# Kernel optimization log

Measured on AMD Instinct MI355X. Metric: run time of the kernel, lower is better.

Reference implementation:

```python
import jax, jax.numpy as jnp
from jax import lax
import numpy as np

# pywt db4 reconstruction lowpass filter (rec_lo); rec_hi derived by QMF relation
DB4_REC_LO = np.array([0.23037781330885523, 0.7148465705525415, 0.6308807679295904,
                       -0.02798376941698385, -0.18703481171888114, 0.030841381835986965,
                       0.032883011666982945, -0.010597401784997278], dtype=np.float32)


def _filters():
    g0 = jnp.asarray(DB4_REC_LO)
    L = g0.shape[0]
    # pywt orthogonal QMF: rec_hi[k] = (-1)^k * rec_lo[L-1-k]
    g1 = ((-1.0) ** jnp.arange(L, dtype=jnp.float32)) * g0[::-1]
    return g0, g1


def _sfb1d(lo, hi, g0, g1, axis):
    """1D synthesis filter bank along `axis`, mode='zero'.
    Equivalent to torch conv_transpose(stride=2, padding=L-2): out_len = 2n - L + 2.
    Implemented as lhs-dilated correlation with the flipped kernel, pad (1,1)."""
    L = g0.shape[0]
    lo = jnp.moveaxis(lo, axis, -1)
    hi = jnp.moveaxis(hi, axis, -1)
    shp = lo.shape
    x0 = lo.reshape(-1, 1, shp[-1])
    x1 = hi.reshape(-1, 1, shp[-1])
    k0 = g0[::-1].reshape(1, 1, L)
    k1 = g1[::-1].reshape(1, 1, L)
    dn = ('NCH', 'OIH', 'NCH')
    y = (lax.conv_general_dilated(x0, k0, (1,), [(1, 1)], lhs_dilation=(2,), dimension_numbers=dn)
         + lax.conv_general_dilated(x1, k1, (1,), [(1, 1)], lhs_dilation=(2,), dimension_numbers=dn))
    y = y.reshape(shp[:-1] + (y.shape[-1],))
    return jnp.moveaxis(y, -1, axis)


def _sfb3d(low, highs, g0, g1):
    # band index bits (bH, bW, bD); band 0 is the lowpass `low`, bands 1..7 from `highs`
    bands = [low] + [highs[:, :, i] for i in range(7)]
    # synthesize along depth (last axis)
    t = [_sfb1d(bands[2 * j], bands[2 * j + 1], g0, g1, -1) for j in range(4)]
    # then along rows (W)
    t = [_sfb1d(t[2 * j], t[2 * j + 1], g0, g1, -2) for j in range(2)]
    # then along cols (H)
    return _sfb1d(t[0], t[1], g0, g1, -3)


def setup_inputs() -> dict:
    key = jax.random.key(0)
    k1, k2, k3 = jax.random.split(key, 3)
    yl = jax.random.normal(k1, (2, 8, 36, 36, 36), dtype=jnp.float32)
    yh0 = jax.random.normal(k2, (2, 8, 7, 66, 66, 66), dtype=jnp.float32)
    yh1 = jax.random.normal(k3, (2, 8, 7, 36, 36, 36), dtype=jnp.float32)
    return {"yl": yl, "yh0": yh0, "yh1": yh1}


def reference(yl, yh0, yh1):
    g0, g1 = _filters()
    ll = yl
    for h in (yh1, yh0):  # coarsest level first (yh reversed)
        # crop ll if one larger than the highpass bands (odd-size handling)
        ll = ll[..., :h.shape[-3], :, :]
        ll = ll[..., :h.shape[-2], :]
        ll = ll[..., :h.shape[-1]]
        ll = _sfb3d(ll, h, g0, g1)
    return ll
```

## Files before the change

kernel.cpp:

```cpp
#include <hip/hip_runtime.h>

__device__ constexpr float G0[8] = {
    0.23037781330885523f,  0.7148465705525415f,  0.6308807679295904f,  -0.02798376941698385f,
    -0.18703481171888114f, 0.030841381835986965f, 0.032883011666982945f, -0.010597401784997278f};
__device__ constexpr float G1[8] = {
    -0.010597401784997278f, -0.032883011666982945f, 0.030841381835986965f, 0.18703481171888114f,
    -0.02798376941698385f,  -0.6308807679295904f,   0.7148465705525415f,  -0.23037781330885523f};

template <int n, int WY>
__global__ __launch_bounds__(256) void idwt3_lds(const float* __restrict__ low,
                                                 const float* __restrict__ highs,
                                                 float* __restrict__ out) {
  constexpr int N = 2 * n - 6;
  constexpr int H = N / 2;
  constexpr int ROWS = WY + 3;
  constexpr int REAL4 = (ROWS * n + 3) / 4;
  constexpr int CH = 4 * REAL4;
  constexpr int TOT4 = 5 * REAL4;
  constexpr int K = (TOT4 + 255) / 256;
  constexpr long n3 = (long)n * n * n;
  constexpr int n3_4 = (int)(n3 / 4);

  __shared__ __align__(16) float slab[5 * CH];

  const int tid = threadIdx.x;
  const int zb0 = blockIdx.x * 2;
  const int yb0 = blockIdx.y * WY;
  const int b = blockIdx.z;
  const int ux = tid % H;
  const int ty = tid / H;
  const bool z1ok = (zb0 + 1) < H;

  const float* const lowv = low + (long)b * n3;
  const float* const highv = highs + (long)b * 7 * n3;

  float4 st[K];

  auto stage_load = [&](int band) {
    const float* src = (band == 0) ? lowv : (highv + (long)(band - 1) * n3);
#pragma unroll
    for (int k = 0; k < K; ++k) {
      const int idx = tid + k * 256;
      if (idx < TOT4) {
        const int dv = idx / REAL4;
        const int c = idx - dv * REAL4;
        const int v = min(zb0 + dv, n - 1);
        int rel4 = ((v * n + yb0) * n) / 4 + c;
        rel4 = min(rel4, n3_4 - 1);
        st[k] = *reinterpret_cast<const float4*>(src + 4 * (long)rel4);
      }
    }
  };

  float acc[4][2][2] = {};

  stage_load(0);

#pragma unroll 1
  for (int band = 0; band < 8; ++band) {
    if (band) __syncthreads();
#pragma unroll
    for (int k = 0; k < K; ++k) {
      const int idx = tid + k * 256;
      if (idx < TOT4) *reinterpret_cast<float4*>(&slab[4 * idx]) = st[k];
    }
    __syncthreads();
    if (band < 7) stage_load(band + 1);

    if (ty < WY) {
      const float* Gx = (band & 1) ? G1 : G0;
      const float* Gy = (band & 2) ? G1 : G0;
      const float* Gz = (band & 4) ? G1 : G0;
#pragma unroll
      for (int dv = 0; dv < 5; ++dv) {
        float d[4][2];
#pragma unroll
        for (int du = 0; du < 4; ++du) {
          const int base = dv * CH + (ty + du) * n + ux;
          const float r0 = slab[base], r1 = slab[base + 1];
          const float r2 = slab[base + 2], r3 = slab[base + 3];
          d[du][0] = r3 * Gx[0] + r2 * Gx[2] + r1 * Gx[4] + r0 * Gx[6];
          d[du][1] = r3 * Gx[1] + r2 * Gx[3] + r1 * Gx[5] + r0 * Gx[7];
        }
        float ey[2][2];
#pragma unroll
        for (int py = 0; py < 2; ++py) {
#pragma unroll
          for (int px = 0; px < 2; ++px) {
            float s = d[0][px] * Gy[py + 6];
            s = fmaf(d[1][px], Gy[py + 4], s);
            s = fmaf(d[2][px], Gy[py + 2], s);
            s = fmaf(d[3][px], Gy[py + 0], s);
            ey[py][px] = s;
          }
        }
#pragma unroll
        for (int zo = 0; zo < 4; ++zo) {
          const int mz = (zo >> 1) + 3 - dv;
          if (mz >= 0 && mz <= 3) {
            const float w = Gz[(zo & 1) + 2 * mz];
#pragma unroll
            for (int py = 0; py < 2; ++py)
#pragma unroll
              for (int px = 0; px < 2; ++px)
                acc[zo][py][px] = fmaf(ey[py][px], w, acc[zo][py][px]);
          }
        }
      }
    }
  }

  const int uy = yb0 + ty;
  if (ty < WY && uy < H) {
    const long N3 = (long)N * N * N;
    float* obase = out + (long)b * N3 + 2 * ux;
#pragma unroll
    for (int zo = 0; zo < 4; ++zo) {
      if (zo >= 2 && !z1ok) continue;
      const int gz = 2 * zb0 + zo;
#pragma unroll
      for (int py = 0; py < 2; ++py) {
        const int gy = 2 * uy + py;
        float2 vv = make_float2(acc[zo][py][0], acc[zo][py][1]);
        *reinterpret_cast<float2*>(obase + ((long)gz * N + gy) * N) = vv;
      }
    }
  }
}

extern "C" void kernel_launch(void* const* d_in, const int* in_sizes, int n_in,
                              void* d_out, int out_size, void* d_ws, size_t ws_size,
                              hipStream_t stream) {
  const float* yl  = nullptr;
  const float* yh0 = nullptr;
  const float* yh1 = nullptr;
  for (int i = 0; i < n_in; ++i) {
    if (in_sizes[i] == 746496)        yl  = (const float*)d_in[i];
    else if (in_sizes[i] == 32199552) yh0 = (const float*)d_in[i];
    else if (in_sizes[i] == 5225472)  yh1 = (const float*)d_in[i];
  }
  if (!yl || !yh0 || !yh1) {
    yl  = (const float*)d_in[0];
    yh0 = (const float*)d_in[1];
    yh1 = (const float*)d_in[2];
  }
  float* out = (float*)d_out;
  float* ll  = (float*)d_ws;

  idwt3_lds<36, 7><<<dim3(17, 5, 16), 256, 0, stream>>>(yl, yh1, ll);

  idwt3_lds<66, 4><<<dim3(32, 16, 16), 256, 0, stream>>>(ll, yh0, out);
}
```

Measured before the change: 516.6 us.

## Separate x-axis synthesis into shared pass pairing lo/hi bands

Bands are now handled in lo/hi pairs along x. A cooperative pass filters each pair along x into a shared intermediate buffer, and the y/z passes then read that buffer instead of redoing the x filter per band. This removes the x-filter work that was repeated for every output row and halves the number of outer band iterations. In exchange it doubles register staging and shared-memory use, which can lower occupancy, and adds an extra barrier per pair. The first-level launch also changes row tiling from 7 to 3 rows per block with more blocks.

```diff
diff --git a/kernel.cpp b/kernel.cpp
--- a/kernel.cpp
+++ b/kernel.cpp
@@ -8,20 +8,25 @@
     -0.02798376941698385f,  -0.6308807679295904f,   0.7148465705525415f,  -0.23037781330885523f};
 
 template <int n, int WY>
-__global__ __launch_bounds__(256) void idwt3_lds(const float* __restrict__ low,
+__global__ __launch_bounds__(256) void idwt3_sep(const float* __restrict__ low,
                                                  const float* __restrict__ highs,
                                                  float* __restrict__ out) {
   constexpr int N = 2 * n - 6;
   constexpr int H = N / 2;
   constexpr int ROWS = WY + 3;
-  constexpr int REAL4 = (ROWS * n + 3) / 4;
+  constexpr int CHF = ROWS * n;
+  constexpr int REAL4 = (CHF + 3) / 4;
   constexpr int CH = 4 * REAL4;
   constexpr int TOT4 = 5 * REAL4;
   constexpr int K = (TOT4 + 255) / 256;
+  constexpr int W2 = 2 * H;
+  constexpr int PTOT = 5 * ROWS * H;
+  constexpr int KX = (PTOT + 255) / 256;
   constexpr long n3 = (long)n * n * n;
   constexpr int n3_4 = (int)(n3 / 4);
 
-  __shared__ __align__(16) float slab[5 * CH];
+  __shared__ __align__(16) float raw[2][5 * CH];
+  __shared__ __align__(16) float xs[5 * ROWS * W2];
 
   const int tid = threadIdx.x;
   const int zb0 = blockIdx.x * 2;
@@ -34,10 +39,11 @@
   const float* const lowv = low + (long)b * n3;
   const float* const highv = highs + (long)b * 7 * n3;
 
-  float4 st[K];
+  float4 st[2][K];
 
-  auto stage_load = [&](int band) {
-    const float* src = (band == 0) ? lowv : (highv + (long)(band - 1) * n3);
+  auto stage_load = [&](int p) {
+    const float* srcL = (p == 0) ? lowv : (highv + (long)(2 * p - 1) * n3);
+    const float* srcH = highv + (long)(2 * p) * n3;
 #pragma unroll
     for (int k = 0; k < K; ++k) {
       const int idx = tid + k * 256;
@@ -47,7 +53,8 @@
         const int v = min(zb0 + dv, n - 1);
         int rel4 = ((v * n + yb0) * n) / 4 + c;
         rel4 = min(rel4, n3_4 - 1);
-        st[k] = *reinterpret_cast<const float4*>(src + 4 * (long)rel4);
+        st[0][k] = *reinterpret_cast<const float4*>(srcL + 4 * (long)rel4);
+        st[1][k] = *reinterpret_cast<const float4*>(srcH + 4 * (long)rel4);
       }
     }
   };
@@ -57,30 +64,53 @@
   stage_load(0);
 
 #pragma unroll 1
-  for (int band = 0; band < 8; ++band) {
-    if (band) __syncthreads();
+  for (int p = 0; p < 4; ++p) {
 #pragma unroll
     for (int k = 0; k < K; ++k) {
       const int idx = tid + k * 256;
-      if (idx < TOT4) *reinterpret_cast<float4*>(&slab[4 * idx]) = st[k];
+      if (idx < TOT4) {
+        *reinterpret_cast<float4*>(&raw[0][4 * idx]) = st[0][k];
+        *reinterpret_cast<float4*>(&raw[1][4 * idx]) = st[1][k];
+      }
     }
     __syncthreads();
-    if (band < 7) stage_load(band + 1);
+    if (p < 3) stage_load(p + 1);
+
+#pragma unroll
+    for (int k = 0; k < KX; ++k) {
+      const int idx = tid + k * 256;
+      if (idx < PTOT) {
+        const int dv = idx / (ROWS * H);
+        const int r = idx - dv * (ROWS * H);
+        const int row = r / H;
+        const int u = r - row * H;
+        const int base = dv * CH + row * n + u;
+        const float l0 = raw[0][base],     l1 = raw[0][base + 1],
+                    l2 = raw[0][base + 2], l3 = raw[0][base + 3];
+        const float h0 = raw[1][base],     h1 = raw[1][base + 1],
+                    h2 = raw[1][base + 2], h3 = raw[1][base + 3];
+        float x0 = l0 * G0[6] + l1 * G0[4] + l2 * G0[2] + l3 * G0[0]
+                 + h0 * G1[6] + h1 * G1[4] + h2 * G1[2] + h3 * G1[0];
+        float x1 = l0 * G0[7] + l1 * G0[5] + l2 * G0[3] + l3 * G0[1]
+                 + h0 * G1[7] + h1 * G1[5] + h2 * G1[3] + h3 * G1[1];
+        *reinterpret_cast<float2*>(&xs[(dv * ROWS + row) * W2 + 2 * u]) =
+            make_float2(x0, x1);
+      }
+    }
+    __syncthreads();
 
     if (ty < WY) {
-      const float* Gx = (band & 1) ? G1 : G0;
-      const float* Gy = (band & 2) ? G1 : G0;
-      const float* Gz = (band & 4) ? G1 : G0;
+      const float* Gy = (p & 1) ? G1 : G0;
+      const float* Gz = (p & 2) ? G1 : G0;
 #pragma unroll
       for (int dv = 0; dv < 5; ++dv) {
         float d[4][2];
 #pragma unroll
         for (int du = 0; du < 4; ++du) {
-          const int base = dv * CH + (ty + du) * n + ux;
-          const float r0 = slab[base], r1 = slab[base + 1];
-          const float r2 = slab[base + 2], r3 = slab[base + 3];
-          d[du][0] = r3 * Gx[0] + r2 * Gx[2] + r1 * Gx[4] + r0 * Gx[6];
-          d[du][1] = r3 * Gx[1] + r2 * Gx[3] + r1 * Gx[5] + r0 * Gx[7];
+          const float2 v2 = *reinterpret_cast<const float2*>(
+              &xs[(dv * ROWS + ty + du) * W2 + 2 * ux]);
+          d[du][0] = v2.x;
+          d[du][1] = v2.y;
         }
         float ey[2][2];
 #pragma unroll
@@ -147,7 +177,7 @@
   float* out = (float*)d_out;
   float* ll  = (float*)d_ws;
 
-  idwt3_lds<36, 7><<<dim3(17, 5, 16), 256, 0, stream>>>(yl, yh1, ll);
+  idwt3_sep<36, 3><<<dim3(17, 11, 16), 256, 0, stream>>>(yl, yh1, ll);
 
-  idwt3_lds<66, 4><<<dim3(32, 16, 16), 256, 0, stream>>>(ll, yh0, out);
+  idwt3_sep<66, 4><<<dim3(32, 16, 16), 256, 0, stream>>>(ll, yh0, out);
 }
```

Result: no change. 524.5 us (+1.5%).
